# Optimization experiments

Hardware: AMD Instinct MI355X
Metric: run time of the kernel (lower is better)

The kernel has to match this reference:

```python
import jax, jax.numpy as jnp
import numpy as np

B, N, C = 8, 1024, 768
H = 12            # num_heads
D = C // H        # head_dim = 64
P = 16            # num_prefix


def setup_inputs() -> dict:
    key = jax.random.key(0)
    ks = jax.random.split(key, 7)
    s = 0.02
    return {
        "x": jax.random.normal(ks[0], (B, N, C), jnp.float32),
        "qkv_w": jax.random.normal(ks[1], (3 * C, C), jnp.float32) * s,
        "qkv_b": jax.random.normal(ks[2], (3 * C,), jnp.float32) * s,
        "proj_w": jax.random.normal(ks[3], (C, C), jnp.float32) * s,
        "proj_b": jax.random.normal(ks[4], (C,), jnp.float32) * s,
        "prefix_k": jax.random.normal(ks[5], (P, C), jnp.float32) * s,
        "prefix_v": jax.random.normal(ks[6], (P, C), jnp.float32) * s,
    }


def reference(x, qkv_w, qkv_b, proj_w, proj_b, prefix_k, prefix_v):
    scale = D ** -0.5
    # qkv projection: [B,N,3C] -> [3,B,H,N,D]
    qkv = (jnp.einsum("bnc,fc->bnf", x, qkv_w) + qkv_b)
    qkv = qkv.reshape(B, N, 3, H, D).transpose(2, 0, 3, 1, 4)
    q, k, v = qkv[0], qkv[1], qkv[2]
    # prefix KV: [P,C] -> [1,H,P,D], broadcast over batch
    pk = prefix_k.reshape(1, P, H, D).transpose(0, 2, 1, 3)
    pv = prefix_v.reshape(1, P, H, D).transpose(0, 2, 1, 3)
    k = jnp.concatenate([jnp.broadcast_to(pk, (B, H, P, D)), k], axis=2)  # [B,H,P+N,D]
    v = jnp.concatenate([jnp.broadcast_to(pv, (B, H, P, D)), v], axis=2)
    # attention: [B,H,N,P+N]
    attn = jnp.einsum("bhnd,bhmd->bhnm", q, k) * scale
    attn = jax.nn.softmax(attn, axis=-1)
    out = jnp.einsum("bhnm,bhmd->bhnd", attn, v)  # [B,H,N,D]
    out = out.transpose(0, 2, 1, 3).reshape(B, N, C)
    out = jnp.einsum("bnc,fc->bnf", out, proj_w) + proj_b
    return out
```

## Files before the change

kernel.cpp:

```cpp
#include <hip/hip_runtime.h>


typedef __attribute__((ext_vector_type(8))) short short8;
typedef __attribute__((ext_vector_type(2))) float f32x2;
typedef __attribute__((ext_vector_type(4))) float f32x4;
typedef __attribute__((ext_vector_type(16))) float f32x16;
typedef __attribute__((ext_vector_type(4))) int i32x4;

#define GLOAD_LDS16(g, l)                                              \
    __builtin_amdgcn_global_load_lds(                                  \
        (const __attribute__((address_space(1))) void*)(g),            \
        (__attribute__((address_space(3))) void*)(l), 16, 0, 0)

#define GBAR  asm volatile("s_barrier" ::: "memory")
#define LGKM0 asm volatile("s_waitcnt lgkmcnt(0)" ::: "memory")
#define VMC0  asm volatile("s_waitcnt vmcnt(0)" ::: "memory")
#define PSWAP(a, b) asm("v_permlane32_swap_b32 %0, %1" : "+v"(a), "+v"(b))

__device__ __forceinline__ unsigned short f2b(float f) {
    unsigned u = __builtin_bit_cast(unsigned, f);
    u = (u + 0x7fffu + ((u >> 16) & 1u)) >> 16;
    return (unsigned short)u;
}

__device__ __forceinline__ int cvt_pk_bf16(float lo, float hi) {
    int r;
    asm("v_cvt_pk_bf16_f32 %0, %1, %2" : "=v"(r) : "v"(lo), "v"(hi));
    return r;
}

__device__ __forceinline__ float fexp2(float x) {
    float r;
    asm("v_exp_f32 %0, %1" : "=v"(r) : "v"(x));
    return r;
}

__global__ void cvt_f32_to_bf16(const float* __restrict__ in,
                                unsigned short* __restrict__ out, int n4) {
    int i = blockIdx.x * blockDim.x + threadIdx.x;
    int stride = gridDim.x * blockDim.x;
    for (; i < n4; i += stride) {
        float4 v = reinterpret_cast<const float4*>(in)[i];
        ushort4 o;
        o.x = f2b(v.x); o.y = f2b(v.y); o.z = f2b(v.z); o.w = f2b(v.w);
        reinterpret_cast<ushort4*>(out)[i] = o;
    }
}

__global__ void prefill(const float* __restrict__ pk, const float* __restrict__ pv,
                        unsigned short* __restrict__ kc, unsigned short* __restrict__ vT) {
    int idx = blockIdx.x * 256 + threadIdx.x;
    int d  = idx & 63;
    int j  = (idx >> 6) & 31;
    int bh = idx >> 11;
    if (bh >= 96) return;
    int h = bh % 12;
    if (j < 16) {
        kc[((size_t)bh * 1056 + j) * 64 + d]  = f2b(pk[j * 768 + h * 64 + d]);
        vT[((size_t)bh * 64 + d) * 1056 + j]  = f2b(pv[j * 768 + h * 64 + d]);
    } else {
        int row = 1040 + (j - 16);
        kc[((size_t)bh * 1056 + row) * 64 + d] = 0;
        vT[((size_t)bh * 64 + d) * 1056 + row] = 0;
    }
}

template<int MODE, int FT>
__global__ __launch_bounds__(256, 4) void gemm_dp(
    const unsigned short* __restrict__ A,
    const unsigned short* __restrict__ W,
    const float* __restrict__ bias,
    int M, int F, int K,
    unsigned short* __restrict__ qbuf,
    unsigned short* __restrict__ kcbuf,
    unsigned short* __restrict__ vtbuf,
    float* __restrict__ fout)
{
    __shared__ __align__(16) unsigned short SH[17472];
#define AS_(s) (SH + (s) * 4096)
#define BS_(s) (SH + 8192 + (s) * 4096)

    const int tid = threadIdx.x;
    const int bid = (blockIdx.x & 7) * (gridDim.x >> 3) + (blockIdx.x >> 3);
    const int m0 = (bid / FT) * 128;
    const int f0 = (bid % FT) * 128;
    const int wid = tid >> 6, lane = tid & 63;
    const int wr = wid >> 1, wc = wid & 1;
    const int lo = lane & 15, hi = lane >> 4;
    const int rdsw = ((hi ^ (lo & 3)) << 4);

#define STG(KT)                                                                  \
    { _Pragma("unroll") for (int r_ = 0; r_ < 2; ++r_) {                         \
        int id_ = r_ * 256 + tid; int row_ = id_ >> 2;                           \
        int sc_ = (((id_ & 3) ^ (row_ & 3)) << 3);                               \
        GLOAD_LDS16(A + (size_t)(m0 + row_) * K + (KT) * 32 + sc_,               \
                    (char*)AS_((KT) & 1) + id_ * 16);                            \
        GLOAD_LDS16(W + (size_t)(f0 + row_) * K + (KT) * 32 + sc_,               \
                    (char*)BS_((KT) & 1) + id_ * 16);                            \
    } }

    f32x4 acc[4][4];
#pragma unroll
    for (int i = 0; i < 4; ++i)
#pragma unroll
        for (int j = 0; j < 4; ++j) acc[i][j] = (f32x4)0.f;

    const int nt = K >> 5;

    STG(0);
    VMC0; GBAR;

    for (int t = 0; t < nt; ++t) {
        const int s = t & 1;
        if (t + 1 < nt) STG(t + 1);

        short8 av[4], bv[4];
#pragma unroll
        for (int i = 0; i < 4; ++i) {
            av[i] = *reinterpret_cast<const short8*>(
                (const char*)AS_(s) + (wr * 64 + i * 16 + lo) * 64 + rdsw);
            bv[i] = *reinterpret_cast<const short8*>(
                (const char*)BS_(s) + (wc * 64 + i * 16 + lo) * 64 + rdsw);
        }
        __builtin_amdgcn_s_setprio(1);
#pragma unroll
        for (int i = 0; i < 4; ++i)
#pragma unroll
            for (int j = 0; j < 4; ++j)
                acc[i][j] = __builtin_amdgcn_mfma_f32_16x16x32_bf16(
                    av[i], bv[j], acc[i][j], 0, 0, 0);
        __builtin_amdgcn_s_setprio(0);

        if (t + 1 < nt) { VMC0; GBAR; }
    }

    if (MODE == 1) {
#pragma unroll
        for (int mi = 0; mi < 4; ++mi) {
#pragma unroll
            for (int ni = 0; ni < 4; ++ni) {
                int f = f0 + wc * 64 + ni * 16 + lo;
                float bv2 = bias[f];
#pragma unroll
                for (int r = 0; r < 4; ++r) {
                    int m = m0 + wr * 64 + mi * 16 + hi * 4 + r;
                    fout[(size_t)m * F + f] = acc[mi][ni][r] + bv2;
                }
            }
        }
    } else {
        __syncthreads();
        const float sc = (f0 < 768) ? 0.1803368801111204f : 1.f;
#pragma unroll
        for (int mi = 0; mi < 4; ++mi) {
#pragma unroll
            for (int ni = 0; ni < 4; ++ni) {
                int fc = wc * 64 + ni * 16 + lo;
                float bv2 = bias[f0 + fc];
#pragma unroll
                for (int r = 0; r < 4; ++r) {
                    int mr = wr * 64 + mi * 16 + hi * 4 + r;
                    SH[mr * 136 + fc] = f2b((acc[mi][ni][r] + bv2) * sc);
                }
            }
        }
        __syncthreads();

        const int row2 = tid >> 1, half = tid & 1;
        const int b_ = m0 >> 10, n0 = m0 & 1023;
        if (f0 < 1536) {
            const unsigned short* src = SH + row2 * 136 + half * 64;
            unsigned short* dst;
            if (f0 < 768) {
                int h = (f0 >> 6) + half;
                dst = qbuf + (((size_t)(b_ * 12 + h) * 1024 + n0 + row2) << 6);
            } else {
                int h = ((f0 - 768) >> 6) + half;
                dst = kcbuf + (((size_t)(b_ * 12 + h) * 1056 + 16 + n0 + row2) << 6);
            }
#pragma unroll
            for (int c = 0; c < 8; ++c)
                *reinterpret_cast<short8*>(dst + c * 8) =
                    *reinterpret_cast<const short8*>(src + c * 8);
        } else {
            int fv = f0 - 1536 + row2;
            int h = fv >> 6, d = fv & 63;
            unsigned short* dst = vtbuf + ((size_t)(b_ * 12 + h) * 64 + d) * 1056
                                  + 16 + n0 + half * 64;
#pragma unroll
            for (int c = 0; c < 8; ++c) {
                short8 v;
#pragma unroll
                for (int j = 0; j < 8; ++j)
                    v[j] = (short)SH[(half * 64 + c * 8 + j) * 136 + row2];
                *reinterpret_cast<short8*>(dst + c * 8) = v;
            }
        }
    }
#undef STG
#undef AS_
#undef BS_
}

__global__ __launch_bounds__(256) void attn_kernel(
    const unsigned short* __restrict__ q,
    const unsigned short* __restrict__ kc,
    const unsigned short* __restrict__ vT,
    unsigned short* __restrict__ ao)
{
    __shared__ __align__(16) unsigned short OT[4][32 * 72];
    __shared__ __align__(16) unsigned short KS[4][2][2048];

    const int tid = threadIdx.x;
    const int w = tid >> 6, lane = tid & 63;
    const int ql = lane & 31;
    const int hi = lane >> 5;

    const int bid = (blockIdx.x & 7) * 96 + (blockIdx.x >> 3);
    const int head = bid >> 3;
    const int qt = (bid & 7) * 4 + w;
    const int b = head / 12, h = head % 12;

    const unsigned short* qp = q + ((size_t)head * 1024 + qt * 32) * 64;
    const unsigned short* kp = kc + (size_t)head * 1056 * 64;
    const unsigned short* vp = vT + (size_t)head * 64 * 1056;

    const int srow = lane >> 3;
    const int sce  = ((lane & 7) ^ srow) << 3;
    const int rsw  = (ql & 7) << 4;

    short8 qf[4];
#pragma unroll
    for (int ks = 0; ks < 4; ++ks)
        qf[ks] = *reinterpret_cast<const short8*>(qp + (size_t)ql * 64 + ks * 16 + hi * 8);

#pragma unroll
    for (int i = 0; i < 4; ++i)
        GLOAD_LDS16(kp + (size_t)(i * 8 + srow) * 64 + sce,
                    (char*)&KS[w][0][0] + i * 1024);

    f32x16 o0 = (f32x16)0.f, o1 = (f32x16)0.f;
    const f32x16 fz = (f32x16)0.f;
    f32x2 l2 = (f32x2)0.f;

    for (int t = 0; t < 33; ++t) {
        const int kbase = t * 32;
        const char* kcur = (const char*)&KS[w][t & 1][0];

        if (t < 32) {
            char* knx = (char*)&KS[w][(t & 1) ^ 1][0];
            const unsigned short* ksrc = kp + (size_t)(kbase + 32) * 64;
#pragma unroll
            for (int i = 0; i < 4; ++i)
                GLOAD_LDS16(ksrc + (size_t)(i * 8 + srow) * 64 + sce, knx + i * 1024);
            asm volatile("s_waitcnt vmcnt(4)" ::: "memory");
        } else {
            asm volatile("s_waitcnt vmcnt(0)" ::: "memory");
        }

        f32x16 s;
        __builtin_amdgcn_s_setprio(1);
        {
            short8 kf = *reinterpret_cast<const short8*>(kcur + ql * 128 + ((hi * 16) ^ rsw));
            s = __builtin_amdgcn_mfma_f32_32x32x16_bf16(kf, qf[0], fz, 0, 0, 0);
        }
#pragma unroll
        for (int ks = 1; ks < 4; ++ks) {
            short8 kf = *reinterpret_cast<const short8*>(
                kcur + ql * 128 + ((ks * 32 + hi * 16) ^ rsw));
            s = __builtin_amdgcn_mfma_f32_32x32x16_bf16(kf, qf[ks], s, 0, 0, 0);
        }
        __builtin_amdgcn_s_setprio(0);

        if (t == 32) {
#pragma unroll
            for (int r = 8; r < 16; ++r) s[r] = -1e30f;
        }

        float p[16];
#pragma unroll
        for (int r = 0; r < 16; ++r) p[r] = fexp2(s[r]);
#pragma unroll
        for (int r = 0; r < 16; r += 2) {
            f32x2 pr; pr[0] = p[r]; pr[1] = p[r + 1];
            l2 += pr;
        }

        int w0 = cvt_pk_bf16(p[0],  p[1]),  w1 = cvt_pk_bf16(p[2],  p[3]);
        int w2 = cvt_pk_bf16(p[4],  p[5]),  w3 = cvt_pk_bf16(p[6],  p[7]);
        int w4 = cvt_pk_bf16(p[8],  p[9]),  w5 = cvt_pk_bf16(p[10], p[11]);
        int w6 = cvt_pk_bf16(p[12], p[13]), w7 = cvt_pk_bf16(p[14], p[15]);
        PSWAP(w0, w2); PSWAP(w1, w3); PSWAP(w4, w6); PSWAP(w5, w7);
        i32x4 pw0, pw1;
        pw0[0] = w0; pw0[1] = w1; pw0[2] = w2; pw0[3] = w3;
        pw1[0] = w4; pw1[1] = w5; pw1[2] = w6; pw1[3] = w7;
        short8 pf0 = __builtin_bit_cast(short8, pw0);
        short8 pf1 = __builtin_bit_cast(short8, pw1);

        short8 vf00 = *reinterpret_cast<const short8*>(vp + (size_t)ql * 1056 + kbase + hi * 8);
        short8 vf01 = *reinterpret_cast<const short8*>(vp + (size_t)ql * 1056 + kbase + 16 + hi * 8);
        short8 vf10 = *reinterpret_cast<const short8*>(vp + (size_t)(32 + ql) * 1056 + kbase + hi * 8);
        short8 vf11 = *reinterpret_cast<const short8*>(vp + (size_t)(32 + ql) * 1056 + kbase + 16 + hi * 8);
        __builtin_amdgcn_s_setprio(1);
        o0 = __builtin_amdgcn_mfma_f32_32x32x16_bf16(vf00, pf0, o0, 0, 0, 0);
        o0 = __builtin_amdgcn_mfma_f32_32x32x16_bf16(vf01, pf1, o0, 0, 0, 0);
        o1 = __builtin_amdgcn_mfma_f32_32x32x16_bf16(vf10, pf0, o1, 0, 0, 0);
        o1 = __builtin_amdgcn_mfma_f32_32x32x16_bf16(vf11, pf1, o1, 0, 0, 0);
        __builtin_amdgcn_s_setprio(0);
    }

    float l = l2[0] + l2[1];
    l += __shfl_xor(l, 32);
    const float rinv = 1.f / l;
    o0 *= rinv;
    o1 *= rinv;
    unsigned short* ow = &OT[w][0];
#pragma unroll
    for (int r = 0; r < 16; r += 2) {
        int d = (r & 3) + 8 * (r >> 2) + 4 * hi;
        unsigned v0 = (unsigned)f2b(o0[r]) | ((unsigned)f2b(o0[r + 1]) << 16);
        *reinterpret_cast<unsigned*>(ow + ql * 72 + d) = v0;
        unsigned v1 = (unsigned)f2b(o1[r]) | ((unsigned)f2b(o1[r + 1]) << 16);
        *reinterpret_cast<unsigned*>(ow + ql * 72 + 32 + d) = v1;
    }
    LGKM0;
    __builtin_amdgcn_sched_barrier(0);
    const int row2 = lane >> 1, half = lane & 1;
    unsigned short* dst = ao + ((size_t)b * 1024 + qt * 32 + row2) * 768 + h * 64 + half * 32;
    const unsigned short* src = ow + row2 * 72 + half * 32;
#pragma unroll
    for (int c = 0; c < 4; ++c)
        *reinterpret_cast<short8*>(dst + c * 8) =
            *reinterpret_cast<const short8*>(src + c * 8);
}

extern "C" void kernel_launch(void* const* d_in, const int* in_sizes, int n_in,
                              void* d_out, int out_size, void* d_ws, size_t ws_size,
                              hipStream_t stream) {
    const float* x        = (const float*)d_in[0];
    const float* qkv_w    = (const float*)d_in[1];
    const float* qkv_b    = (const float*)d_in[2];
    const float* proj_w   = (const float*)d_in[3];
    const float* proj_b   = (const float*)d_in[4];
    const float* prefix_k = (const float*)d_in[5];
    const float* prefix_v = (const float*)d_in[6];
    float* out = (float*)d_out;

    char* ws = (char*)d_ws;
    unsigned short* xb   = (unsigned short*)(ws);
    unsigned short* wqkv = (unsigned short*)(ws + 12582912);
    unsigned short* wp   = (unsigned short*)(ws + 16121856);
    unsigned short* qb   = (unsigned short*)(ws + 17301504);
    unsigned short* kcb  = (unsigned short*)(ws + 29884416);
    unsigned short* vtb  = (unsigned short*)(ws + 42860544);
    unsigned short* aob  = xb;

    cvt_f32_to_bf16<<<1024, 256, 0, stream>>>(x, xb, 8192 * 768 / 4);
    cvt_f32_to_bf16<<<512, 256, 0, stream>>>(qkv_w, wqkv, 2304 * 768 / 4);
    cvt_f32_to_bf16<<<256, 256, 0, stream>>>(proj_w, wp, 768 * 768 / 4);
    prefill<<<768, 256, 0, stream>>>(prefix_k, prefix_v, kcb, vtb);

    gemm_dp<0, 18><<<1152, 256, 0, stream>>>(xb, wqkv, qkv_b, 8192, 2304, 768,
                                             qb, kcb, vtb, nullptr);
    attn_kernel<<<768, 256, 0, stream>>>(qb, kcb, vtb, aob);
    gemm_dp<1, 6><<<384, 256, 0, stream>>>(aob, wp, proj_b, 8192, 768, 768,
                                           nullptr, nullptr, nullptr, out);
}
```

Measured before the change: 136.0 us.

## Triple-buffer GEMM LDS staging with two tiles of prefetch in flight

The bf16 GEMM mainloop moves from a double-buffered to a triple-buffered LDS ring. It now issues global-to-LDS loads two k-tiles ahead and waits with vmcnt(4) instead of vmcnt(0), so one tile's loads stay in flight during the MFMA work. Shared memory per block grows, so the launch bound drops from 4 to 3 blocks per SM, trading occupancy for deeper prefetch.

```diff
diff --git a/kernel.cpp b/kernel.cpp
--- a/kernel.cpp
+++ b/kernel.cpp
@@ -14,6 +14,7 @@
 
 #define GBAR  asm volatile("s_barrier" ::: "memory")
 #define LGKM0 asm volatile("s_waitcnt lgkmcnt(0)" ::: "memory")
+#define VMC4  asm volatile("s_waitcnt vmcnt(4)" ::: "memory")
 #define VMC0  asm volatile("s_waitcnt vmcnt(0)" ::: "memory")
 #define PSWAP(a, b) asm("v_permlane32_swap_b32 %0, %1" : "+v"(a), "+v"(b))
 
@@ -66,7 +67,7 @@
 }
 
 template<int MODE, int FT>
-__global__ __launch_bounds__(256, 4) void gemm_dp(
+__global__ __launch_bounds__(256, 3) void gemm_dp(
     const unsigned short* __restrict__ A,
     const unsigned short* __restrict__ W,
     const float* __restrict__ bias,
@@ -76,9 +77,9 @@
     unsigned short* __restrict__ vtbuf,
     float* __restrict__ fout)
 {
-    __shared__ __align__(16) unsigned short SH[17472];
+    __shared__ __align__(16) unsigned short SH[24576];
 #define AS_(s) (SH + (s) * 4096)
-#define BS_(s) (SH + 8192 + (s) * 4096)
+#define BS_(s) (SH + 12288 + (s) * 4096)
 
     const int tid = threadIdx.x;
     const int bid = (blockIdx.x & 7) * (gridDim.x >> 3) + (blockIdx.x >> 3);
@@ -89,14 +90,14 @@
     const int lo = lane & 15, hi = lane >> 4;
     const int rdsw = ((hi ^ (lo & 3)) << 4);
 
-#define STG(KT)                                                                  \
+#define STG(SLOT, KT)                                                            \
     { _Pragma("unroll") for (int r_ = 0; r_ < 2; ++r_) {                         \
         int id_ = r_ * 256 + tid; int row_ = id_ >> 2;                           \
         int sc_ = (((id_ & 3) ^ (row_ & 3)) << 3);                               \
         GLOAD_LDS16(A + (size_t)(m0 + row_) * K + (KT) * 32 + sc_,               \
-                    (char*)AS_((KT) & 1) + id_ * 16);                            \
+                    (char*)AS_(SLOT) + id_ * 16);                                \
         GLOAD_LDS16(W + (size_t)(f0 + row_) * K + (KT) * 32 + sc_,               \
-                    (char*)BS_((KT) & 1) + id_ * 16);                            \
+                    (char*)BS_(SLOT) + id_ * 16);                                \
     } }
 
     f32x4 acc[4][4];
@@ -107,21 +108,27 @@
 
     const int nt = K >> 5;
 
-    STG(0);
-    VMC0; GBAR;
-
+    STG(0, 0);
+    STG(1, 1);
+    VMC4; GBAR;
+
+    int slot = 0, nslot = 2;
     for (int t = 0; t < nt; ++t) {
-        const int s = t & 1;
-        if (t + 1 < nt) STG(t + 1);
+        if (t + 2 < nt) {
+            STG(nslot, t + 2);
+            nslot = (nslot == 2) ? 0 : nslot + 1;
+        }
 
         short8 av[4], bv[4];
 #pragma unroll
         for (int i = 0; i < 4; ++i) {
             av[i] = *reinterpret_cast<const short8*>(
-                (const char*)AS_(s) + (wr * 64 + i * 16 + lo) * 64 + rdsw);
+                (const char*)AS_(slot) + (wr * 64 + i * 16 + lo) * 64 + rdsw);
             bv[i] = *reinterpret_cast<const short8*>(
-                (const char*)BS_(s) + (wc * 64 + i * 16 + lo) * 64 + rdsw);
-        }
+                (const char*)BS_(slot) + (wc * 64 + i * 16 + lo) * 64 + rdsw);
+        }
+        slot = (slot == 2) ? 0 : slot + 1;
+
         __builtin_amdgcn_s_setprio(1);
 #pragma unroll
         for (int i = 0; i < 4; ++i)
@@ -131,7 +138,11 @@
                     av[i], bv[j], acc[i][j], 0, 0, 0);
         __builtin_amdgcn_s_setprio(0);
 
-        if (t + 1 < nt) { VMC0; GBAR; }
+        if (t + 1 < nt) {
+            if (t + 2 < nt) { VMC4; }
+            else            { VMC0; }
+            GBAR;
+        }
     }
 
     if (MODE == 1) {
```

Result: faster. 132.3 us (-2.7%).
